# Kernel tuning notes

Hardware: AMD Instinct MI355X
Metric: run time of the kernel (lower is better)

The kernel has to match this reference:

```python
import jax, jax.numpy as jnp
import numpy as np

N = 50000          # nb_nodes
DEG = 32           # avg degree -> every node has DEG outgoing edges (rows covered)
E = N * DEG        # 1,600,000 edges
F_IN = 512
F_OUT = 256


def setup_inputs() -> dict:
    key = jax.random.key(0)
    k = jax.random.split(key, 8)
    x = jax.random.normal(k[0], (1, N, F_IN), dtype=jnp.float32)
    W = jax.random.normal(k[1], (F_IN, F_OUT), dtype=jnp.float32) * 0.05
    a1_w = jax.random.normal(k[2], (F_OUT, 1), dtype=jnp.float32) * 0.05
    a1_b = jnp.zeros((1,), jnp.float32)
    a2_w = jax.random.normal(k[3], (F_OUT, 1), dtype=jnp.float32) * 0.05
    a2_b = jnp.zeros((1,), jnp.float32)
    bias_out = jnp.zeros((F_OUT,), jnp.float32)
    # edge list: each node has exactly DEG neighbors (rows sorted, all rows present)
    edge_row = jnp.repeat(jnp.arange(N, dtype=jnp.int32), DEG)
    edge_col = jax.random.randint(k[4], (E,), 0, N, dtype=jnp.int32)
    bias_vals = jnp.ones((E,), jnp.float32)  # SparseTensor values of bias_mat
    return {"x": x, "W": W, "a1_w": a1_w, "a1_b": a1_b, "a2_w": a2_w,
            "a2_b": a2_b, "bias_out": bias_out, "bias_vals": bias_vals,
            "edge_row": edge_row, "edge_col": edge_col}


def reference(x, W, a1_w, a1_b, a2_w, a2_b, bias_out, bias_vals, edge_row, edge_col):
    # conv1d(k=1, no bias): per-node linear projection. x: [1, N, F_IN]
    seq = jnp.einsum('nf,fo->no', x[0], W)                 # [N, F_OUT]
    f1 = (seq @ a1_w + a1_b)[:, 0]                         # [N]
    f2 = (seq @ a2_w + a2_b)[:, 0]                         # [N]
    # sparse_add(bias_mat*f1_row, bias_mat^T-style*f2_col) -> per-edge logits
    e = bias_vals * f1[edge_row] + bias_vals * f2[edge_col]  # [E]
    e = jax.nn.leaky_relu(e, negative_slope=0.2)
    # sparse_softmax: softmax over nonzero entries of each row
    row_max = jax.ops.segment_max(e, edge_row, num_segments=N)
    row_max = jnp.where(jnp.isfinite(row_max), row_max, 0.0)
    ee = jnp.exp(e - row_max[edge_row])
    denom = jax.ops.segment_sum(ee, edge_row, num_segments=N)
    coefs = ee / jnp.maximum(denom[edge_row], 1e-30)        # [E]
    # SpMM: out[i] = sum_j coefs[ij] * seq[j]
    vals = jax.ops.segment_sum(coefs[:, None] * seq[edge_col], edge_row,
                               num_segments=N)             # [N, F_OUT]
    ret = jax.nn.elu(vals + bias_out)[None]                # [1, N, F_OUT]
    return ret
```

## Files before the change

kernel.cpp:

```cpp
#include <hip/hip_runtime.h>
#include <stdint.h>

#define N_NODES 50000
#define DEG 32
#define FIN 512
#define FOUT 256

typedef __attribute__((ext_vector_type(4))) float f32x4;
typedef __attribute__((ext_vector_type(8))) short short8;
typedef _Float16 h16x4 __attribute__((ext_vector_type(4)));

__device__ __forceinline__ unsigned short f2bf(float f) {
    union { float f; unsigned int u; } v; v.f = f;
    unsigned int u = v.u;
    return (unsigned short)((u + 0x7FFFu + ((u >> 16) & 1u)) >> 16);
}
__device__ __forceinline__ unsigned short f2h(float f) {
    union { _Float16 h; unsigned short u; } v; v.h = (_Float16)f;
    return v.u;
}

__device__ __forceinline__ void gll16(const void* g, void* l) {
    __builtin_amdgcn_global_load_lds(
        (const __attribute__((address_space(1))) unsigned int*)g,
        (__attribute__((address_space(3))) unsigned int*)(uintptr_t)l,
        16, 0, 0);
}

__global__ void k_wt(const float* __restrict__ W, unsigned short* __restrict__ Wt) {
    int idx = blockIdx.x * 256 + threadIdx.x;
    int c = idx >> 9;
    int k = idx & 511;
    Wt[idx] = f2bf(W[k * FOUT + c]);
}

#define GBM 64
#define GBK 64

__global__ __launch_bounds__(512, 4)
void k_gemm(const float* __restrict__ x, const unsigned short* __restrict__ Wt,
            unsigned short* __restrict__ seqh) {
    __shared__ unsigned short As[8 * 512];
    __shared__ unsigned short Bs[32 * 512];

    const int tid  = threadIdx.x;
    const int lane = tid & 63;
    const int w    = tid >> 6;
    const int row0 = blockIdx.x * GBM;
    const int fr   = lane & 15;
    const int fq   = lane >> 4;

    const int af = w >> 1, as_ = w & 1;
    int arow = row0 + af * 16 + fr;
    if (arow >= N_NODES) arow = N_NODES - 1;
    const float* aptr = x + (size_t)arow * FIN + as_ * 32 + fq * 8;
    unsigned short* awr = &As[(w << 9) + lane * 8];

    const unsigned short* bsrc[4];
    unsigned short* bdst[4];
#pragma unroll
    for (int c = 0; c < 4; c++) {
        int frag = w * 4 + c;
        int n16 = frag >> 1, bs_ = frag & 1;
        bsrc[c] = Wt + (size_t)(n16 * 16 + fr) * FIN + bs_ * 32 + fq * 8;
        bdst[c] = &Bs[frag << 9];
    }

    const int mf0 = (w >> 2) * 2;
    const int nc0 = (w & 3) * 4;

    f32x4 acc[2][4];
    f32x4 zero4 = {0.f, 0.f, 0.f, 0.f};
#pragma unroll
    for (int i = 0; i < 2; i++)
#pragma unroll
        for (int j = 0; j < 4; j++) acc[i][j] = zero4;

    float4 p0 = *(const float4*)(aptr);
    float4 p1 = *(const float4*)(aptr + 4);
#pragma unroll
    for (int c = 0; c < 4; c++) gll16(bsrc[c], bdst[c]);
    {
        ushort4 lo = { f2bf(p0.x), f2bf(p0.y), f2bf(p0.z), f2bf(p0.w) };
        ushort4 hi = { f2bf(p1.x), f2bf(p1.y), f2bf(p1.z), f2bf(p1.w) };
        *(ushort4*)(awr)     = lo;
        *(ushort4*)(awr + 4) = hi;
    }
    __syncthreads();

    for (int t = 0; t < 8; ++t) {
        float4 q0 = p0, q1 = p1;
        if (t < 7) {
            q0 = *(const float4*)(aptr + (t + 1) * GBK);
            q1 = *(const float4*)(aptr + (t + 1) * GBK + 4);
        }
#pragma unroll
        for (int s = 0; s < 2; ++s) {
            short8 a0 = *(const short8*)(const void*)&As[((mf0 + 0) * 2 + s) * 512 + lane * 8];
            short8 a1 = *(const short8*)(const void*)&As[((mf0 + 1) * 2 + s) * 512 + lane * 8];
            short8 b0 = *(const short8*)(const void*)&Bs[((nc0 + 0) * 2 + s) * 512 + lane * 8];
            short8 b1 = *(const short8*)(const void*)&Bs[((nc0 + 1) * 2 + s) * 512 + lane * 8];
            short8 b2 = *(const short8*)(const void*)&Bs[((nc0 + 2) * 2 + s) * 512 + lane * 8];
            short8 b3 = *(const short8*)(const void*)&Bs[((nc0 + 3) * 2 + s) * 512 + lane * 8];
            acc[0][0] = __builtin_amdgcn_mfma_f32_16x16x32_bf16(a0, b0, acc[0][0], 0, 0, 0);
            acc[0][1] = __builtin_amdgcn_mfma_f32_16x16x32_bf16(a0, b1, acc[0][1], 0, 0, 0);
            acc[0][2] = __builtin_amdgcn_mfma_f32_16x16x32_bf16(a0, b2, acc[0][2], 0, 0, 0);
            acc[0][3] = __builtin_amdgcn_mfma_f32_16x16x32_bf16(a0, b3, acc[0][3], 0, 0, 0);
            acc[1][0] = __builtin_amdgcn_mfma_f32_16x16x32_bf16(a1, b0, acc[1][0], 0, 0, 0);
            acc[1][1] = __builtin_amdgcn_mfma_f32_16x16x32_bf16(a1, b1, acc[1][1], 0, 0, 0);
            acc[1][2] = __builtin_amdgcn_mfma_f32_16x16x32_bf16(a1, b2, acc[1][2], 0, 0, 0);
            acc[1][3] = __builtin_amdgcn_mfma_f32_16x16x32_bf16(a1, b3, acc[1][3], 0, 0, 0);
        }
        if (t < 7) {
            __syncthreads();
            int kk = (t + 1) * GBK;
#pragma unroll
            for (int c = 0; c < 4; c++) gll16(bsrc[c] + kk, bdst[c]);
            ushort4 lo = { f2bf(q0.x), f2bf(q0.y), f2bf(q0.z), f2bf(q0.w) };
            ushort4 hi = { f2bf(q1.x), f2bf(q1.y), f2bf(q1.z), f2bf(q1.w) };
            *(ushort4*)(awr)     = lo;
            *(ushort4*)(awr + 4) = hi;
            __syncthreads();
        }
    }

    const int m0 = (w >> 2) * 32, n0 = (w & 3) * 64;
#pragma unroll
    for (int mi = 0; mi < 2; mi++) {
#pragma unroll
        for (int r = 0; r < 4; r++) {
            int row = row0 + m0 + mi * 16 + fq * 4 + r;
            if (row < N_NODES) {
#pragma unroll
                for (int ni = 0; ni < 4; ni++) {
                    int col = n0 + ni * 16 + fr;
                    seqh[(size_t)row * FOUT + col] = f2h(acc[mi][ni][r]);
                }
            }
        }
    }
}

__global__ __launch_bounds__(256, 4)
void k_prep(const unsigned short* __restrict__ seqh,
            const float* __restrict__ a1w, const float* __restrict__ a1b,
            const float* __restrict__ a2w, const float* __restrict__ a2b,
            float* __restrict__ f1, float* __restrict__ f2,
            unsigned int* __restrict__ seq8, float* __restrict__ scale) {
    int node = (blockIdx.x * 256 + threadIdx.x) >> 6;
    int lane = threadIdx.x & 63;
    h16x4 s = *(const h16x4*)(const void*)(seqh + (size_t)node * FOUT + lane * 4);
    float4 w1 = *(const float4*)(a1w + lane * 4);
    float4 w2 = *(const float4*)(a2w + lane * 4);
    float v0 = (float)s[0], v1 = (float)s[1], v2 = (float)s[2], v3 = (float)s[3];
    float d1 = v0 * w1.x + v1 * w1.y + v2 * w1.z + v3 * w1.w;
    float d2 = v0 * w2.x + v1 * w2.y + v2 * w2.z + v3 * w2.w;
    float am = fmaxf(fmaxf(fabsf(v0), fabsf(v1)), fmaxf(fabsf(v2), fabsf(v3)));
#pragma unroll
    for (int off = 32; off; off >>= 1) {
        d1 += __shfl_xor(d1, off, 64);
        d2 += __shfl_xor(d2, off, 64);
        am = fmaxf(am, __shfl_xor(am, off, 64));
    }
    am = fmaxf(am, 1e-8f);
    float inv = 127.0f / am;
    int q0 = (int)rintf(v0 * inv);
    int q1 = (int)rintf(v1 * inv);
    int q2 = (int)rintf(v2 * inv);
    int q3 = (int)rintf(v3 * inv);
    unsigned int packed = (q0 & 255) | ((q1 & 255) << 8) |
                          ((q2 & 255) << 16) | ((unsigned int)(q3 & 255) << 24);
    seq8[(size_t)node * 64 + lane] = packed;
    if (lane == 0) {
        scale[node] = am * (1.0f / 127.0f);
        f1[node] = d1 + a1b[0];
        f2[node] = d2 + a2b[0];
    }
}

#define LOADS(J) \
    int   c##J = __shfl(col,  (J), 64); \
    float w##J = __shfl(coef, (J), 64); \
    int   v##J = *(const int*)(const void*)(sp + (size_t)c##J * FOUT);

#define ACCUM(J) \
    a0 += w##J * (float)((v##J << 24) >> 24); \
    a1 += w##J * (float)((v##J << 16) >> 24); \
    a2 += w##J * (float)((v##J <<  8) >> 24); \
    a3 += w##J * (float)( v##J        >> 24);

__global__ __launch_bounds__(256, 4)
void k_attn(const char* __restrict__ seq8, const float* __restrict__ scale,
            const float* __restrict__ f1, const float* __restrict__ f2,
            const float* __restrict__ bias_vals,
            const int* __restrict__ edge_col,
            const float* __restrict__ bias_out,
            float* __restrict__ out) {
    const int lane = threadIdx.x & 63;
    const int node = (blockIdx.x * 256 + threadIdx.x) >> 6;

    float e = -1e30f;
    int col = 0;
    float sc = 0.f;
    if (lane < 32) {
        int eidx = node * DEG + lane;
        col = edge_col[eidx];
        sc  = scale[col];
        float bv = bias_vals[eidx];
        e = bv * f1[node] + bv * f2[col];
        e = (e >= 0.f) ? e : 0.2f * e;
    }
    float m = e;
#pragma unroll
    for (int off = 16; off; off >>= 1) m = fmaxf(m, __shfl_xor(m, off, 32));
    float p = __expf(e - m);
    float s = p;
#pragma unroll
    for (int off = 16; off; off >>= 1) s += __shfl_xor(s, off, 32);
    float coef = (p / s) * sc;

    const char* sp = seq8 + lane * 4;
    float a0 = 0.f, a1 = 0.f, a2 = 0.f, a3 = 0.f;
    {
        LOADS(0) LOADS(1) LOADS(2) LOADS(3) LOADS(4) LOADS(5) LOADS(6) LOADS(7)
        ACCUM(0) ACCUM(1) ACCUM(2) ACCUM(3) ACCUM(4) ACCUM(5) ACCUM(6) ACCUM(7)
    }
    {
        LOADS(8) LOADS(9) LOADS(10) LOADS(11) LOADS(12) LOADS(13) LOADS(14) LOADS(15)
        ACCUM(8) ACCUM(9) ACCUM(10) ACCUM(11) ACCUM(12) ACCUM(13) ACCUM(14) ACCUM(15)
    }
    {
        LOADS(16) LOADS(17) LOADS(18) LOADS(19) LOADS(20) LOADS(21) LOADS(22) LOADS(23)
        ACCUM(16) ACCUM(17) ACCUM(18) ACCUM(19) ACCUM(20) ACCUM(21) ACCUM(22) ACCUM(23)
    }
    {
        LOADS(24) LOADS(25) LOADS(26) LOADS(27) LOADS(28) LOADS(29) LOADS(30) LOADS(31)
        ACCUM(24) ACCUM(25) ACCUM(26) ACCUM(27) ACCUM(28) ACCUM(29) ACCUM(30) ACCUM(31)
    }

    int fbase = lane * 4;
    float4 bo = *(const float4*)(bias_out + fbase);
    float4 r;
    r.x = a0 + bo.x; r.y = a1 + bo.y; r.z = a2 + bo.z; r.w = a3 + bo.w;
    r.x = (r.x > 0.f) ? r.x : expm1f(r.x);
    r.y = (r.y > 0.f) ? r.y : expm1f(r.y);
    r.z = (r.z > 0.f) ? r.z : expm1f(r.z);
    r.w = (r.w > 0.f) ? r.w : expm1f(r.w);
    *(float4*)(out + (size_t)node * FOUT + fbase) = r;
}

extern "C" void kernel_launch(void* const* d_in, const int* in_sizes, int n_in,
                              void* d_out, int out_size, void* d_ws, size_t ws_size,
                              hipStream_t stream) {
    const float* x         = (const float*)d_in[0];
    const float* W         = (const float*)d_in[1];
    const float* a1w       = (const float*)d_in[2];
    const float* a1b       = (const float*)d_in[3];
    const float* a2w       = (const float*)d_in[4];
    const float* a2b       = (const float*)d_in[5];
    const float* bias_out  = (const float*)d_in[6];
    const float* bias_vals = (const float*)d_in[7];
    const int* edge_col    = (const int*)d_in[9];
    float* out = (float*)d_out;

    char* ws = (char*)d_ws;
    unsigned short* Wt   = (unsigned short*)ws;
    unsigned short* seqh = (unsigned short*)(ws + 262144);
    float* f1    = (float*)(ws + 262144 + 25600000);
    float* f2    = (float*)(ws + 262144 + 25600000 + 200064);
    float* scale = (float*)(ws + 262144 + 25600000 + 2 * 200064);
    unsigned int* seq8 = (unsigned int*)(ws + 262144 + 25600000 + 3 * 200064);

    hipLaunchKernelGGL(k_wt,   dim3(512), dim3(256), 0, stream, W, Wt);
    hipLaunchKernelGGL(k_gemm, dim3((N_NODES + GBM - 1) / GBM), dim3(512), 0, stream,
                       x, Wt, seqh);
    hipLaunchKernelGGL(k_prep, dim3(N_NODES / 4), dim3(256), 0, stream,
                       seqh, a1w, a1b, a2w, a2b, f1, f2, seq8, scale);
    hipLaunchKernelGGL(k_attn, dim3(N_NODES / 4), dim3(256), 0, stream,
                       (const char*)seq8, scale, f1, f2, bias_vals, edge_col,
                       bias_out, out);
}
```

Baseline: 126.0 us.

## Fuse attention-prep and int8 quantization into GEMM epilogue with double-buffered LDS

Removes the separate k_prep kernel and the fp16 seq intermediate. The GEMM epilogue now computes the f1/f2 dot products and the per-row absmax through shuffles and LDS, then quantizes and writes int8 seq directly, with a permuted feature order that k_attn's output store undoes. It also double-buffers the A/B LDS tiles so the next k-slice loads are issued before the MFMAs, dropping one barrier per iteration. In exchange LDS use doubles and launch bounds drop to 2 blocks per CU, which may lower occupancy, and quantization is now done from fp32 accumulators rather than fp16.

```diff
diff --git a/kernel.cpp b/kernel.cpp
--- a/kernel.cpp
+++ b/kernel.cpp
@@ -8,16 +8,11 @@
 
 typedef __attribute__((ext_vector_type(4))) float f32x4;
 typedef __attribute__((ext_vector_type(8))) short short8;
-typedef _Float16 h16x4 __attribute__((ext_vector_type(4)));
 
 __device__ __forceinline__ unsigned short f2bf(float f) {
     union { float f; unsigned int u; } v; v.f = f;
     unsigned int u = v.u;
     return (unsigned short)((u + 0x7FFFu + ((u >> 16) & 1u)) >> 16);
-}
-__device__ __forceinline__ unsigned short f2h(float f) {
-    union { _Float16 h; unsigned short u; } v; v.h = (_Float16)f;
-    return v.u;
 }
 
 __device__ __forceinline__ void gll16(const void* g, void* l) {
@@ -37,11 +32,14 @@
 #define GBM 64
 #define GBK 64
 
-__global__ __launch_bounds__(512, 4)
+__global__ __launch_bounds__(512, 2)
 void k_gemm(const float* __restrict__ x, const unsigned short* __restrict__ Wt,
-            unsigned short* __restrict__ seqh) {
-    __shared__ unsigned short As[8 * 512];
-    __shared__ unsigned short Bs[32 * 512];
+            const float* __restrict__ a1w, const float* __restrict__ a1b,
+            const float* __restrict__ a2w, const float* __restrict__ a2b,
+            float* __restrict__ f1, float* __restrict__ f2,
+            float* __restrict__ scale, unsigned int* __restrict__ seq8) {
+    __shared__ unsigned short As[2][8 * 512];
+    __shared__ unsigned short Bs[2][32 * 512];
 
     const int tid  = threadIdx.x;
     const int lane = tid & 63;
@@ -54,20 +52,22 @@
     int arow = row0 + af * 16 + fr;
     if (arow >= N_NODES) arow = N_NODES - 1;
     const float* aptr = x + (size_t)arow * FIN + as_ * 32 + fq * 8;
-    unsigned short* awr = &As[(w << 9) + lane * 8];
+    const int awoff = (w << 9) + lane * 8;
 
     const unsigned short* bsrc[4];
-    unsigned short* bdst[4];
+    int boff[4];
 #pragma unroll
     for (int c = 0; c < 4; c++) {
         int frag = w * 4 + c;
         int n16 = frag >> 1, bs_ = frag & 1;
         bsrc[c] = Wt + (size_t)(n16 * 16 + fr) * FIN + bs_ * 32 + fq * 8;
-        bdst[c] = &Bs[frag << 9];
+        boff[c] = frag << 9;
     }
 
     const int mf0 = (w >> 2) * 2;
     const int nc0 = (w & 3) * 4;
+    const int mg = w >> 2, ng = w & 3;
+    const int n0 = ng * 64;
 
     f32x4 acc[2][4];
     f32x4 zero4 = {0.f, 0.f, 0.f, 0.f};
@@ -76,32 +76,36 @@
 #pragma unroll
         for (int j = 0; j < 4; j++) acc[i][j] = zero4;
 
-    float4 p0 = *(const float4*)(aptr);
-    float4 p1 = *(const float4*)(aptr + 4);
-#pragma unroll
-    for (int c = 0; c < 4; c++) gll16(bsrc[c], bdst[c]);
-    {
+#pragma unroll
+    for (int c = 0; c < 4; c++) gll16(bsrc[c], &Bs[0][boff[c]]);
+    {
+        float4 p0 = *(const float4*)(aptr);
+        float4 p1 = *(const float4*)(aptr + 4);
         ushort4 lo = { f2bf(p0.x), f2bf(p0.y), f2bf(p0.z), f2bf(p0.w) };
         ushort4 hi = { f2bf(p1.x), f2bf(p1.y), f2bf(p1.z), f2bf(p1.w) };
-        *(ushort4*)(awr)     = lo;
-        *(ushort4*)(awr + 4) = hi;
+        *(ushort4*)&As[0][awoff]     = lo;
+        *(ushort4*)&As[0][awoff + 4] = hi;
     }
     __syncthreads();
 
     for (int t = 0; t < 8; ++t) {
-        float4 q0 = p0, q1 = p1;
+        const int rb = t & 1, wb = rb ^ 1;
+        float4 q0, q1;
         if (t < 7) {
-            q0 = *(const float4*)(aptr + (t + 1) * GBK);
-            q1 = *(const float4*)(aptr + (t + 1) * GBK + 4);
+            int kk = (t + 1) * GBK;
+#pragma unroll
+            for (int c = 0; c < 4; c++) gll16(bsrc[c] + kk, &Bs[wb][boff[c]]);
+            q0 = *(const float4*)(aptr + kk);
+            q1 = *(const float4*)(aptr + kk + 4);
         }
 #pragma unroll
         for (int s = 0; s < 2; ++s) {
-            short8 a0 = *(const short8*)(const void*)&As[((mf0 + 0) * 2 + s) * 512 + lane * 8];
-            short8 a1 = *(const short8*)(const void*)&As[((mf0 + 1) * 2 + s) * 512 + lane * 8];
-            short8 b0 = *(const short8*)(const void*)&Bs[((nc0 + 0) * 2 + s) * 512 + lane * 8];
-            short8 b1 = *(const short8*)(const void*)&Bs[((nc0 + 1) * 2 + s) * 512 + lane * 8];
-            short8 b2 = *(const short8*)(const void*)&Bs[((nc0 + 2) * 2 + s) * 512 + lane * 8];
-            short8 b3 = *(const short8*)(const void*)&Bs[((nc0 + 3) * 2 + s) * 512 + lane * 8];
+            short8 a0 = *(const short8*)(const void*)&As[rb][((mf0 + 0) * 2 + s) * 512 + lane * 8];
+            short8 a1 = *(const short8*)(const void*)&As[rb][((mf0 + 1) * 2 + s) * 512 + lane * 8];
+            short8 b0 = *(const short8*)(const void*)&Bs[rb][((nc0 + 0) * 2 + s) * 512 + lane * 8];
+            short8 b1 = *(const short8*)(const void*)&Bs[rb][((nc0 + 1) * 2 + s) * 512 + lane * 8];
+            short8 b2 = *(const short8*)(const void*)&Bs[rb][((nc0 + 2) * 2 + s) * 512 + lane * 8];
+            short8 b3 = *(const short8*)(const void*)&Bs[rb][((nc0 + 3) * 2 + s) * 512 + lane * 8];
             acc[0][0] = __builtin_amdgcn_mfma_f32_16x16x32_bf16(a0, b0, acc[0][0], 0, 0, 0);
             acc[0][1] = __builtin_amdgcn_mfma_f32_16x16x32_bf16(a0, b1, acc[0][1], 0, 0, 0);
             acc[0][2] = __builtin_amdgcn_mfma_f32_16x16x32_bf16(a0, b2, acc[0][2], 0, 0, 0);
@@ -112,69 +116,85 @@
             acc[1][3] = __builtin_amdgcn_mfma_f32_16x16x32_bf16(a1, b3, acc[1][3], 0, 0, 0);
         }
         if (t < 7) {
-            __syncthreads();
-            int kk = (t + 1) * GBK;
-#pragma unroll
-            for (int c = 0; c < 4; c++) gll16(bsrc[c] + kk, bdst[c]);
             ushort4 lo = { f2bf(q0.x), f2bf(q0.y), f2bf(q0.z), f2bf(q0.w) };
             ushort4 hi = { f2bf(q1.x), f2bf(q1.y), f2bf(q1.z), f2bf(q1.w) };
-            *(ushort4*)(awr)     = lo;
-            *(ushort4*)(awr + 4) = hi;
+            *(ushort4*)&As[wb][awoff]     = lo;
+            *(ushort4*)&As[wb][awoff + 4] = hi;
             __syncthreads();
         }
     }
 
-    const int m0 = (w >> 2) * 32, n0 = (w & 3) * 64;
+    __syncthreads();
+    float* f1p_l  = (float*)(void*)As;
+    float* f2p_l  = f1p_l + 256;
+    float* am_l   = f2p_l + 256;
+    float* finv_l = am_l + 256;
+
+    const float w10 = a1w[n0 + fr],      w11 = a1w[n0 + 16 + fr];
+    const float w12 = a1w[n0 + 32 + fr], w13 = a1w[n0 + 48 + fr];
+    const float w20 = a2w[n0 + fr],      w21 = a2w[n0 + 16 + fr];
+    const float w22 = a2w[n0 + 32 + fr], w23 = a2w[n0 + 48 + fr];
+
 #pragma unroll
     for (int mi = 0; mi < 2; mi++) {
 #pragma unroll
         for (int r = 0; r < 4; r++) {
-            int row = row0 + m0 + mi * 16 + fq * 4 + r;
-            if (row < N_NODES) {
-#pragma unroll
-                for (int ni = 0; ni < 4; ni++) {
-                    int col = n0 + ni * 16 + fr;
-                    seqh[(size_t)row * FOUT + col] = f2h(acc[mi][ni][r]);
-                }
+            float c0 = acc[mi][0][r], c1 = acc[mi][1][r];
+            float c2 = acc[mi][2][r], c3 = acc[mi][3][r];
+            float s1 = c0 * w10 + c1 * w11 + c2 * w12 + c3 * w13;
+            float s2 = c0 * w20 + c1 * w21 + c2 * w22 + c3 * w23;
+            float am = fmaxf(fmaxf(fabsf(c0), fabsf(c1)),
+                             fmaxf(fabsf(c2), fabsf(c3)));
+#pragma unroll
+            for (int off = 1; off < 16; off <<= 1) {
+                s1 += __shfl_xor(s1, off, 64);
+                s2 += __shfl_xor(s2, off, 64);
+                am = fmaxf(am, __shfl_xor(am, off, 64));
             }
-        }
-    }
-}
-
-__global__ __launch_bounds__(256, 4)
-void k_prep(const unsigned short* __restrict__ seqh,
-            const float* __restrict__ a1w, const float* __restrict__ a1b,
-            const float* __restrict__ a2w, const float* __restrict__ a2b,
-            float* __restrict__ f1, float* __restrict__ f2,
-            unsigned int* __restrict__ seq8, float* __restrict__ scale) {
-    int node = (blockIdx.x * 256 + threadIdx.x) >> 6;
-    int lane = threadIdx.x & 63;
-    h16x4 s = *(const h16x4*)(const void*)(seqh + (size_t)node * FOUT + lane * 4);
-    float4 w1 = *(const float4*)(a1w + lane * 4);
-    float4 w2 = *(const float4*)(a2w + lane * 4);
-    float v0 = (float)s[0], v1 = (float)s[1], v2 = (float)s[2], v3 = (float)s[3];
-    float d1 = v0 * w1.x + v1 * w1.y + v2 * w1.z + v3 * w1.w;
-    float d2 = v0 * w2.x + v1 * w2.y + v2 * w2.z + v3 * w2.w;
-    float am = fmaxf(fmaxf(fabsf(v0), fabsf(v1)), fmaxf(fabsf(v2), fabsf(v3)));
-#pragma unroll
-    for (int off = 32; off; off >>= 1) {
-        d1 += __shfl_xor(d1, off, 64);
-        d2 += __shfl_xor(d2, off, 64);
-        am = fmaxf(am, __shfl_xor(am, off, 64));
-    }
-    am = fmaxf(am, 1e-8f);
-    float inv = 127.0f / am;
-    int q0 = (int)rintf(v0 * inv);
-    int q1 = (int)rintf(v1 * inv);
-    int q2 = (int)rintf(v2 * inv);
-    int q3 = (int)rintf(v3 * inv);
-    unsigned int packed = (q0 & 255) | ((q1 & 255) << 8) |
-                          ((q2 & 255) << 16) | ((unsigned int)(q3 & 255) << 24);
-    seq8[(size_t)node * 64 + lane] = packed;
-    if (lane == 0) {
-        scale[node] = am * (1.0f / 127.0f);
-        f1[node] = d1 + a1b[0];
-        f2[node] = d2 + a2b[0];
+            if (fr == 0) {
+                int rowb = mg * 32 + mi * 16 + fq * 4 + r;
+                f1p_l[rowb * 4 + ng] = s1;
+                f2p_l[rowb * 4 + ng] = s2;
+                am_l[rowb * 4 + ng]  = am;
+            }
+        }
+    }
+    __syncthreads();
+
+    if (tid < 64) {
+        float4 p1 = *(const float4*)&f1p_l[tid * 4];
+        float4 p2 = *(const float4*)&f2p_l[tid * 4];
+        float4 pm = *(const float4*)&am_l[tid * 4];
+        float s1 = p1.x + p1.y + p1.z + p1.w + a1b[0];
+        float s2 = p2.x + p2.y + p2.z + p2.w + a2b[0];
+        float am = fmaxf(fmaxf(pm.x, pm.y), fmaxf(pm.z, pm.w));
+        am = fmaxf(am, 1e-8f);
+        int grow = row0 + tid;
+        if (grow < N_NODES) {
+            f1[grow] = s1;
+            f2[grow] = s2;
+            scale[grow] = am * (1.0f / 127.0f);
+        }
+        finv_l[tid] = 127.0f / am;
+    }
+    __syncthreads();
+
+#pragma unroll
+    for (int mi = 0; mi < 2; mi++) {
+#pragma unroll
+        for (int r = 0; r < 4; r++) {
+            int rowb = mg * 32 + mi * 16 + fq * 4 + r;
+            int grow = row0 + rowb;
+            float inv = finv_l[rowb];
+            int q0 = ((int)rintf(acc[mi][0][r] * inv)) & 255;
+            int q1 = ((int)rintf(acc[mi][1][r] * inv)) & 255;
+            int q2 = ((int)rintf(acc[mi][2][r] * inv)) & 255;
+            int q3 = ((int)rintf(acc[mi][3][r] * inv)) & 255;
+            unsigned int pk = (unsigned int)q0 | ((unsigned int)q1 << 8) |
+                              ((unsigned int)q2 << 16) | ((unsigned int)q3 << 24);
+            if (grow < N_NODES)
+                seq8[(size_t)grow * 64 + ng * 16 + fr] = pk;
+        }
     }
 }
 
@@ -238,15 +258,19 @@
         ACCUM(24) ACCUM(25) ACCUM(26) ACCUM(27) ACCUM(28) ACCUM(29) ACCUM(30) ACCUM(31)
     }
 
-    int fbase = lane * 4;
-    float4 bo = *(const float4*)(bias_out + fbase);
-    float4 r;
-    r.x = a0 + bo.x; r.y = a1 + bo.y; r.z = a2 + bo.z; r.w = a3 + bo.w;
-    r.x = (r.x > 0.f) ? r.x : expm1f(r.x);
-    r.y = (r.y > 0.f) ? r.y : expm1f(r.y);
-    r.z = (r.z > 0.f) ? r.z : expm1f(r.z);
-    r.w = (r.w > 0.f) ? r.w : expm1f(r.w);
-    *(float4*)(out + (size_t)node * FOUT + fbase) = r;
+    const int fb = (lane >> 4) * 64 + (lane & 15);
+    float b0 = bias_out[fb], b1 = bias_out[fb + 16];
+    float b2 = bias_out[fb + 32], b3 = bias_out[fb + 48];
+    float r0 = a0 + b0, r1 = a1 + b1, r2 = a2 + b2, r3 = a3 + b3;
+    r0 = (r0 > 0.f) ? r0 : expm1f(r0);
+    r1 = (r1 > 0.f) ? r1 : expm1f(r1);
+    r2 = (r2 > 0.f) ? r2 : expm1f(r2);
+    r3 = (r3 > 0.f) ? r3 : expm1f(r3);
+    float* op = out + (size_t)node * FOUT + fb;
+    op[0]  = r0;
+    op[16] = r1;
+    op[32] = r2;
+    op[48] = r3;
 }
 
 extern "C" void kernel_launch(void* const* d_in, const int* in_sizes, int n_in,
@@ -264,18 +288,15 @@
     float* out = (float*)d_out;
 
     char* ws = (char*)d_ws;
-    unsigned short* Wt   = (unsigned short*)ws;
-    unsigned short* seqh = (unsigned short*)(ws + 262144);
-    float* f1    = (float*)(ws + 262144 + 25600000);
-    float* f2    = (float*)(ws + 262144 + 25600000 + 200064);
-    float* scale = (float*)(ws + 262144 + 25600000 + 2 * 200064);
-    unsigned int* seq8 = (unsigned int*)(ws + 262144 + 25600000 + 3 * 200064);
+    unsigned short* Wt = (unsigned short*)ws;
+    float* f1    = (float*)(ws + 262144);
+    float* f2    = (float*)(ws + 262144 + 200064);
+    float* scale = (float*)(ws + 262144 + 2 * 200064);
+    unsigned int* seq8 = (unsigned int*)(ws + 262144 + 3 * 200064);
 
     hipLaunchKernelGGL(k_wt,   dim3(512), dim3(256), 0, stream, W, Wt);
     hipLaunchKernelGGL(k_gemm, dim3((N_NODES + GBM - 1) / GBM), dim3(512), 0, stream,
-                       x, Wt, seqh);
-    hipLaunchKernelGGL(k_prep, dim3(N_NODES / 4), dim3(256), 0, stream,
-                       seqh, a1w, a1b, a2w, a2b, f1, f2, seq8, scale);
+                       x, Wt, a1w, a1b, a2w, a2b, f1, f2, scale, seq8);
     hipLaunchKernelGGL(k_attn, dim3(N_NODES / 4), dim3(256), 0, stream,
                        (const char*)seq8, scale, f1, f2, bias_vals, edge_col,
                        bias_out, out);
```

Result: faster. 117.8 us (-6.5%).
